# Optimization experiments

Measured on AMD Instinct MI355X. Metric: run time of the kernel, lower is better.

## Reference

```python
import jax, jax.numpy as jnp
import numpy as np

THRESHOLD = 1.0
DECAY = 0.9


def setup_inputs() -> dict:
    key = jax.random.key(0)
    ks = jax.random.split(key, 7)
    B, D_in, H, D_out = 512, 1024, 2048, 1024
    return {
        "x": jax.random.normal(ks[0], (B, D_in), dtype=jnp.float32),
        "W0": jax.random.normal(ks[1], (H, D_in), dtype=jnp.float32) * 0.03,
        "b0": jax.random.normal(ks[2], (H,), dtype=jnp.float32) * 0.03,
        "W1": jax.random.normal(ks[3], (H, H), dtype=jnp.float32) * 0.03,
        "b1": jax.random.normal(ks[4], (H,), dtype=jnp.float32) * 0.03,
        "W2": jax.random.normal(ks[5], (D_out, H), dtype=jnp.float32) * 0.03,
        "b2": jax.random.normal(ks[6], (D_out,), dtype=jnp.float32) * 0.03,
        "time_steps": 50,
    }


def _lif_layer(layer_input, W, b, time_steps):
    # layer_input is constant over time in the original module, so the
    # per-neuron Linear is computed ONCE as a single matmul.
    I = layer_input @ W.T + b  # [B, out_dim] input current, fixed per step
    V0 = jnp.zeros_like(I)

    def step(V, _):
        V = V * DECAY + I
        s = (V > THRESHOLD).astype(I.dtype)
        V = V * (1.0 - s)
        return V, s

    _, spikes = jax.lax.scan(step, V0, None, length=time_steps)  # [T, B, out]
    spikes = jnp.transpose(spikes, (1, 2, 0))  # [B, out, T]
    return spikes


def reference(x, W0, b0, W1, b1, W2, b2, time_steps):
    s0 = _lif_layer(x, W0, b0, time_steps)
    s1 = _lif_layer(s0.mean(axis=2), W1, b1, time_steps)
    s2 = _lif_layer(s1.mean(axis=2), W2, b2, time_steps)
    # matches (layer_outputs[-1], all_spikes)
    return (s2, s0, s1, s2)
```

## Files before the change

kernel.cpp:

```cpp
#include <hip/hip_runtime.h>

typedef unsigned long long u64;
typedef unsigned int u32;

constexpr int TPB = 256;
constexpr int T  = 50;
constexpr int M  = 512;

__global__ __launch_bounds__(TPB)
void gemm_part(const float* __restrict__ A, const int K, const int N,
               const float* __restrict__ W, float* __restrict__ pp)
{
    constexpr int BM2 = 128, BN2 = 64, BK = 64;
    __shared__ float sA[BK][BM2 + 4];
    __shared__ float sB[BK][BN2 + 4];

    const int tid = threadIdx.x;
    const int tx  = tid & 15;
    const int ty  = tid >> 4;
    const int n0  = blockIdx.x * BN2;
    const int m0  = blockIdx.y * BM2;
    const int kbase = blockIdx.z * 512;

    const int ar = tid >> 1, aks = (tid & 1) << 5;
    const int wr = tid >> 2, wks = (tid & 3) << 4;

    float S[8][4];
    #pragma unroll
    for (int i = 0; i < 8; ++i)
        #pragma unroll
        for (int j = 0; j < 4; ++j) S[i][j] = 0.0f;

    const float* aP = A + (size_t)(m0 + ar) * K + kbase + aks;
    const float* wP = W + (size_t)(n0 + wr) * K + kbase + wks;

    float4 fa[8], fw[4];
    auto loadA = [&](int t) {
        #pragma unroll
        for (int c = 0; c < 8; ++c)
            fa[c] = *reinterpret_cast<const float4*>(aP + t * BK + 4 * c);
    };
    auto loadW = [&](int t) {
        #pragma unroll
        for (int c = 0; c < 4; ++c)
            fw[c] = *reinterpret_cast<const float4*>(wP + t * BK + 4 * c);
    };

    constexpr int NT = 512 / BK;
    loadA(0); loadW(0);

    for (int t = 0; t < NT; ++t) {
        __syncthreads();
        #pragma unroll
        for (int c = 0; c < 8; ++c) {
            sA[aks + 4 * c + 0][ar] = fa[c].x;
            sA[aks + 4 * c + 1][ar] = fa[c].y;
            sA[aks + 4 * c + 2][ar] = fa[c].z;
            sA[aks + 4 * c + 3][ar] = fa[c].w;
        }
        #pragma unroll
        for (int c = 0; c < 4; ++c) {
            sB[wks + 4 * c + 0][wr] = fw[c].x;
            sB[wks + 4 * c + 1][wr] = fw[c].y;
            sB[wks + 4 * c + 2][wr] = fw[c].z;
            sB[wks + 4 * c + 3][wr] = fw[c].w;
        }
        __syncthreads();

        if (t + 1 < NT) { loadA(t + 1); loadW(t + 1); }

        #pragma unroll
        for (int kk = 0; kk < BK; ++kk) {
            const float4 a0 = *reinterpret_cast<const float4*>(&sA[kk][ty * 8]);
            const float4 a1 = *reinterpret_cast<const float4*>(&sA[kk][ty * 8 + 4]);
            const float4 b4 = *reinterpret_cast<const float4*>(&sB[kk][tx * 4]);
            const float a[8] = {a0.x, a0.y, a0.z, a0.w, a1.x, a1.y, a1.z, a1.w};
            const float b[4] = {b4.x, b4.y, b4.z, b4.w};
            #pragma unroll
            for (int i = 0; i < 8; ++i)
                #pragma unroll
                for (int j = 0; j < 4; ++j)
                    S[i][j] = __fmaf_rn(a[i], b[j], S[i][j]);
        }
    }

    float* dst = pp + (size_t)blockIdx.z * M * N;
    #pragma unroll
    for (int i = 0; i < 8; ++i) {
        const size_t off = (size_t)(m0 + ty * 8 + i) * N + (n0 + tx * 4);
        *reinterpret_cast<float4*>(dst + off) =
            make_float4(S[i][0], S[i][1], S[i][2], S[i][3]);
    }
}

template<bool DUP, bool WMEAN>
__global__ __launch_bounds__(TPB)
void merge_lif_expand(const float* __restrict__ pp, const int nchain,
                      const int N, const float* __restrict__ bias,
                      float* __restrict__ meanOut, float* __restrict__ out,
                      float* __restrict__ dup)
{
    __shared__ u64 lm[TPB];
    const int tid = threadIdx.x;
    const size_t base = (size_t)blockIdx.x * TPB;
    const size_t idx  = base + tid;
    const size_t cs   = (size_t)M * N;

    float s = pp[idx];
    for (int c = 1; c < nchain; ++c) s = __fadd_rn(s, pp[(size_t)c * cs + idx]);
    const float I = __fadd_rn(s, bias[idx & (size_t)(N - 1)]);

    float V = 0.0f; u64 msk = 0ull;
    #pragma unroll 1
    for (int t = 0; t < T; ++t) {
        V = __fadd_rn(__fmul_rn(V, 0.9f), I);
        if (V > 1.0f) { V = 0.0f; msk |= (1ull << t); }
    }
    if constexpr (WMEAN)
        meanOut[idx] = __fdiv_rn((float)__popcll(msk), 50.0f);
    lm[tid] = msk;
    __syncthreads();

    constexpr int TOTQ = TPB * T / 4;
    for (int q4 = tid; q4 < TOTQ; q4 += TPB) {
        const int q = q4 << 2;
        int nn = q / T;
        int tt = q - nn * T;
        u64 mk = lm[nn];
        float vals[4];
        #pragma unroll
        for (int c = 0; c < 4; ++c) {
            if (tt >= T) { tt -= T; ++nn; mk = lm[nn]; }
            vals[c] = (float)((mk >> tt) & 1ull);
            ++tt;
        }
        const float4 v4 = make_float4(vals[0], vals[1], vals[2], vals[3]);
        const size_t off = base * T + q;
        *reinterpret_cast<float4*>(out + off) = v4;
        if constexpr (DUP) *reinterpret_cast<float4*>(dup + off) = v4;
    }
}

template<bool IN_MASK>
__global__ __launch_bounds__(TPB)
void lif_gemm_mask(const void* __restrict__ Ain, const int K, const int N,
                   const float* __restrict__ W, const float* __restrict__ bias,
                   u64* __restrict__ maskOut)
{
    constexpr int BM = 64, BN = 64, BK = 64;
    __shared__ float sA[BK][BM + 4];
    __shared__ float sB[BK][BN + 4];
    const int tid = threadIdx.x;
    const int tx = tid & 15, ty = tid >> 4;
    const int n0 = blockIdx.x * BN, m0 = blockIdx.y * BM;
    const int lr = tid >> 2, klc = (tid & 3) << 4;

    float S[4][4], Ia[4][4];
    #pragma unroll
    for (int i = 0; i < 4; ++i)
        #pragma unroll
        for (int j = 0; j < 4; ++j) { S[i][j] = 0.0f; Ia[i][j] = 0.0f; }

    const float* aF = (const float*)Ain + (size_t)(m0 + lr) * K + klc;
    const u64*   aM = (const u64*)Ain   + (size_t)(m0 + lr) * K + klc;
    const float* wp = W + (size_t)(n0 + lr) * K + klc;
    float4 fa[4]; uint4 ma[8]; float4 fw[4];

    auto loadA = [&](int k0) {
        if constexpr (IN_MASK) {
            const uint4* p = reinterpret_cast<const uint4*>(aM + k0);
            #pragma unroll
            for (int c = 0; c < 8; ++c) ma[c] = p[c];
        } else {
            #pragma unroll
            for (int c = 0; c < 4; ++c)
                fa[c] = *reinterpret_cast<const float4*>(aF + k0 + 4 * c);
        }
    };
    auto loadW = [&](int k0) {
        #pragma unroll
        for (int c = 0; c < 4; ++c)
            fw[c] = *reinterpret_cast<const float4*>(wp + k0 + 4 * c);
    };

    const int NT = K / BK;
    loadA(0); loadW(0);
    for (int t = 0; t < NT; ++t) {
        __syncthreads();
        if constexpr (IN_MASK) {
            #pragma unroll
            for (int i = 0; i < 16; ++i) {
                const u32 lo = (i & 1) ? ma[i >> 1].z : ma[i >> 1].x;
                const u32 hi = (i & 1) ? ma[i >> 1].w : ma[i >> 1].y;
                sA[klc + i][lr] = __fdiv_rn((float)(__popc(lo) + __popc(hi)), 50.0f);
            }
        } else {
            #pragma unroll
            for (int c = 0; c < 4; ++c) {
                sA[klc + 4 * c + 0][lr] = fa[c].x;
                sA[klc + 4 * c + 1][lr] = fa[c].y;
                sA[klc + 4 * c + 2][lr] = fa[c].z;
                sA[klc + 4 * c + 3][lr] = fa[c].w;
            }
        }
        #pragma unroll
        for (int c = 0; c < 4; ++c) {
            sB[klc + 4 * c + 0][lr] = fw[c].x;
            sB[klc + 4 * c + 1][lr] = fw[c].y;
            sB[klc + 4 * c + 2][lr] = fw[c].z;
            sB[klc + 4 * c + 3][lr] = fw[c].w;
        }
        __syncthreads();
        if (t + 1 < NT) { loadA((t + 1) * BK); loadW((t + 1) * BK); }
        #pragma unroll
        for (int kk = 0; kk < BK; ++kk) {
            const float4 a4 = *reinterpret_cast<const float4*>(&sA[kk][ty * 4]);
            const float4 b4 = *reinterpret_cast<const float4*>(&sB[kk][tx * 4]);
            const float a[4] = {a4.x, a4.y, a4.z, a4.w};
            const float b[4] = {b4.x, b4.y, b4.z, b4.w};
            #pragma unroll
            for (int i = 0; i < 4; ++i)
                #pragma unroll
                for (int j = 0; j < 4; ++j)
                    S[i][j] = __fmaf_rn(a[i], b[j], S[i][j]);
        }
        if ((((t + 1) * BK) & 511) == 0) {
            #pragma unroll
            for (int i = 0; i < 4; ++i)
                #pragma unroll
                for (int j = 0; j < 4; ++j) {
                    Ia[i][j] = __fadd_rn(Ia[i][j], S[i][j]);
                    S[i][j]  = 0.0f;
                }
        }
    }
    #pragma unroll
    for (int i = 0; i < 4; ++i)
        #pragma unroll
        for (int j = 0; j < 4; ++j) {
            const int mi = ty * 4 + i, nj = tx * 4 + j;
            const float I = __fadd_rn(Ia[i][j], bias[n0 + nj]);
            float V = 0.0f; u64 msk = 0ull;
            #pragma unroll 1
            for (int t = 0; t < T; ++t) {
                V = __fadd_rn(__fmul_rn(V, 0.9f), I);
                if (V > 1.0f) { V = 0.0f; msk |= (1ull << t); }
            }
            maskOut[(size_t)(m0 + mi) * N + (n0 + nj)] = msk;
        }
}

template<bool DUP>
__global__ __launch_bounds__(TPB)
void expand_spikes(const u64* __restrict__ mask, float* __restrict__ out,
                   float* __restrict__ dup)
{
    __shared__ u64 lm[TPB];
    const int tid = threadIdx.x;
    const size_t base = (size_t)blockIdx.x * TPB;
    lm[tid] = mask[base + tid];
    __syncthreads();
    constexpr int TOTQ = TPB * T / 4;
    for (int q4 = tid; q4 < TOTQ; q4 += TPB) {
        const int q = q4 << 2;
        int nn = q / T, tt = q - nn * T;
        u64 mk = lm[nn];
        float vals[4];
        #pragma unroll
        for (int c = 0; c < 4; ++c) {
            if (tt >= T) { tt -= T; ++nn; mk = lm[nn]; }
            vals[c] = (float)((mk >> tt) & 1ull);
            ++tt;
        }
        const float4 v4 = make_float4(vals[0], vals[1], vals[2], vals[3]);
        const size_t off = base * T + q;
        *reinterpret_cast<float4*>(out + off) = v4;
        if constexpr (DUP) *reinterpret_cast<float4*>(dup + off) = v4;
    }
}

extern "C" void kernel_launch(void* const* d_in, const int* in_sizes, int n_in,
                              void* d_out, int out_size, void* d_ws, size_t ws_size,
                              hipStream_t stream) {
    const float* x  = (const float*)d_in[0];
    const float* W0 = (const float*)d_in[1];
    const float* b0 = (const float*)d_in[2];
    const float* W1 = (const float*)d_in[3];
    const float* b1 = (const float*)d_in[4];
    const float* W2 = (const float*)d_in[5];
    const float* b2 = (const float*)d_in[6];
    float* out = (float*)d_out;

    constexpr int H = 2048, DOUT = 1024;
    const size_t s2sz = (size_t)M * DOUT * T;
    const size_t s0sz = (size_t)M * H * T;
    const size_t NH = (size_t)M * H;
    const size_t ND = (size_t)M * DOUT;

    float* s2a = out;
    float* s0  = out + s2sz;
    float* s1  = s0 + s0sz;
    float* s2b = s1 + s0sz;

    dim3 blk(TPB);
    const size_t WS_NEED = (2 * NH + 4 * NH + 4 * ND + 2 * NH) * sizeof(float);

    if (ws_size >= WS_NEED) {
        float* pp0   = (float*)d_ws;
        float* pp1   = pp0 + 2 * NH;
        float* pp2   = pp1 + 4 * NH;
        float* mean0 = pp2 + 4 * ND;
        float* mean1 = mean0 + NH;

        gemm_part<<<dim3(H / 64, M / 128, 2), blk, 0, stream>>>(
            x, 1024, H, W0, pp0);
        merge_lif_expand<false, true><<<(int)(NH / TPB), blk, 0, stream>>>(
            pp0, 2, H, b0, mean0, s0, nullptr);
        gemm_part<<<dim3(H / 64, M / 128, 4), blk, 0, stream>>>(
            mean0, H, H, W1, pp1);
        merge_lif_expand<false, true><<<(int)(NH / TPB), blk, 0, stream>>>(
            pp1, 4, H, b1, mean1, s1, nullptr);
        gemm_part<<<dim3(DOUT / 64, M / 128, 4), blk, 0, stream>>>(
            mean1, H, DOUT, W2, pp2);
        merge_lif_expand<true, false><<<(int)(ND / TPB), blk, 0, stream>>>(
            pp2, 4, DOUT, b2, nullptr, s2b, s2a);
    } else {
        u64* mask0 = (u64*)s1;
        u64* mask1 = (u64*)s2a;
        u64* mask2 = (u64*)d_ws;
        dim3 gH(H / 64, M / 64), gD(DOUT / 64, M / 64);
        lif_gemm_mask<false><<<gH, blk, 0, stream>>>(x, 1024, H, W0, b0, mask0);
        lif_gemm_mask<true ><<<gH, blk, 0, stream>>>(mask0, H, H, W1, b1, mask1);
        lif_gemm_mask<true ><<<gD, blk, 0, stream>>>(mask1, H, DOUT, W2, b2, mask2);
        expand_spikes<false><<<(int)(NH / TPB), blk, 0, stream>>>(mask0, s0, nullptr);
        expand_spikes<false><<<(int)(NH / TPB), blk, 0, stream>>>(mask1, s1, nullptr);
        expand_spikes<true ><<<(int)(ND / TPB), blk, 0, stream>>>(mask2, s2b, s2a);
    }
}
```

Before: 267.1 us.

## Overlap spike expansion writes with next layer GEMM in one combined launch

```diff
diff --git a/kernel.cpp b/kernel.cpp
--- a/kernel.cpp
+++ b/kernel.cpp
@@ -7,104 +7,135 @@
 constexpr int T  = 50;
 constexpr int M  = 512;
 
+template<bool DUP>
 __global__ __launch_bounds__(TPB)
-void gemm_part(const float* __restrict__ A, const int K, const int N,
-               const float* __restrict__ W, float* __restrict__ pp)
+void gemm_expand(const float* __restrict__ A, const int K, const int N,
+                 const float* __restrict__ W, float* __restrict__ pp,
+                 const int gemmBlocks, const int gx, const int gy,
+                 const u64* __restrict__ mask, float* __restrict__ out,
+                 float* __restrict__ dup)
 {
-    constexpr int BM2 = 128, BN2 = 64, BK = 64;
-    __shared__ float sA[BK][BM2 + 4];
-    __shared__ float sB[BK][BN2 + 4];
+    __shared__ float sA[64][128 + 4];
+    __shared__ float sB[64][64 + 4];
+    __shared__ u64   lm[TPB];
 
     const int tid = threadIdx.x;
-    const int tx  = tid & 15;
-    const int ty  = tid >> 4;
-    const int n0  = blockIdx.x * BN2;
-    const int m0  = blockIdx.y * BM2;
-    const int kbase = blockIdx.z * 512;
-
-    const int ar = tid >> 1, aks = (tid & 1) << 5;
-    const int wr = tid >> 2, wks = (tid & 3) << 4;
-
-    float S[8][4];
-    #pragma unroll
-    for (int i = 0; i < 8; ++i)
-        #pragma unroll
-        for (int j = 0; j < 4; ++j) S[i][j] = 0.0f;
-
-    const float* aP = A + (size_t)(m0 + ar) * K + kbase + aks;
-    const float* wP = W + (size_t)(n0 + wr) * K + kbase + wks;
-
-    float4 fa[8], fw[4];
-    auto loadA = [&](int t) {
-        #pragma unroll
-        for (int c = 0; c < 8; ++c)
-            fa[c] = *reinterpret_cast<const float4*>(aP + t * BK + 4 * c);
-    };
-    auto loadW = [&](int t) {
-        #pragma unroll
-        for (int c = 0; c < 4; ++c)
-            fw[c] = *reinterpret_cast<const float4*>(wP + t * BK + 4 * c);
-    };
-
-    constexpr int NT = 512 / BK;
-    loadA(0); loadW(0);
-
-    for (int t = 0; t < NT; ++t) {
+    const int bid = blockIdx.x;
+
+    if (bid < gemmBlocks) {
+        const int x = bid % gx;
+        const int r = bid / gx;
+        const int y = r % gy;
+        const int z = r / gy;
+
+        const int tx = tid & 15;
+        const int ty = tid >> 4;
+        const int n0 = x * 64;
+        const int m0 = y * 128;
+        const int kbase = z * 512;
+
+        const int ar = tid >> 1, aks = (tid & 1) << 5;
+        const int wr = tid >> 2, wks = (tid & 3) << 4;
+
+        float S[8][4];
+        #pragma unroll
+        for (int i = 0; i < 8; ++i)
+            #pragma unroll
+            for (int j = 0; j < 4; ++j) S[i][j] = 0.0f;
+
+        const float* aP = A + (size_t)(m0 + ar) * K + kbase + aks;
+        const float* wP = W + (size_t)(n0 + wr) * K + kbase + wks;
+
+        float4 fa[8], fw[4];
+        auto loadA = [&](int t) {
+            #pragma unroll
+            for (int c = 0; c < 8; ++c)
+                fa[c] = *reinterpret_cast<const float4*>(aP + t * 64 + 4 * c);
+        };
+        auto loadW = [&](int t) {
+            #pragma unroll
+            for (int c = 0; c < 4; ++c)
+                fw[c] = *reinterpret_cast<const float4*>(wP + t * 64 + 4 * c);
+        };
+
+        constexpr int NT = 512 / 64;
+        loadA(0); loadW(0);
+
+        for (int t = 0; t < NT; ++t) {
+            __syncthreads();
+            #pragma unroll
+            for (int c = 0; c < 8; ++c) {
+                sA[aks + 4 * c + 0][ar] = fa[c].x;
+                sA[aks + 4 * c + 1][ar] = fa[c].y;
+                sA[aks + 4 * c + 2][ar] = fa[c].z;
+                sA[aks + 4 * c + 3][ar] = fa[c].w;
+            }
+            #pragma unroll
+            for (int c = 0; c < 4; ++c) {
+                sB[wks + 4 * c + 0][wr] = fw[c].x;
+                sB[wks + 4 * c + 1][wr] = fw[c].y;
+                sB[wks + 4 * c + 2][wr] = fw[c].z;
+                sB[wks + 4 * c + 3][wr] = fw[c].w;
+            }
+            __syncthreads();
+
+            if (t + 1 < NT) { loadA(t + 1); loadW(t + 1); }
+
+            #pragma unroll
+            for (int kk = 0; kk < 64; ++kk) {
+                const float4 a0 = *reinterpret_cast<const float4*>(&sA[kk][ty * 8]);
+                const float4 a1 = *reinterpret_cast<const float4*>(&sA[kk][ty * 8 + 4]);
+                const float4 b4 = *reinterpret_cast<const float4*>(&sB[kk][tx * 4]);
+                const float a[8] = {a0.x, a0.y, a0.z, a0.w, a1.x, a1.y, a1.z, a1.w};
+                const float b[4] = {b4.x, b4.y, b4.z, b4.w};
+                #pragma unroll
+                for (int i = 0; i < 8; ++i)
+                    #pragma unroll
+                    for (int j = 0; j < 4; ++j)
+                        S[i][j] = __fmaf_rn(a[i], b[j], S[i][j]);
+            }
+        }
+
+        float* dst = pp + (size_t)z * M * N;
+        #pragma unroll
+        for (int i = 0; i < 8; ++i) {
+            const size_t off = (size_t)(m0 + ty * 8 + i) * N + (n0 + tx * 4);
+            *reinterpret_cast<float4*>(dst + off) =
+                make_float4(S[i][0], S[i][1], S[i][2], S[i][3]);
+        }
+    } else {
+        const size_t base = (size_t)(bid - gemmBlocks) * TPB;
+        lm[tid] = mask[base + tid];
         __syncthreads();
-        #pragma unroll
-        for (int c = 0; c < 8; ++c) {
-            sA[aks + 4 * c + 0][ar] = fa[c].x;
-            sA[aks + 4 * c + 1][ar] = fa[c].y;
-            sA[aks + 4 * c + 2][ar] = fa[c].z;
-            sA[aks + 4 * c + 3][ar] = fa[c].w;
-        }
-        #pragma unroll
-        for (int c = 0; c < 4; ++c) {
-            sB[wks + 4 * c + 0][wr] = fw[c].x;
-            sB[wks + 4 * c + 1][wr] = fw[c].y;
-            sB[wks + 4 * c + 2][wr] = fw[c].z;
-            sB[wks + 4 * c + 3][wr] = fw[c].w;
-        }
-        __syncthreads();
-
-        if (t + 1 < NT) { loadA(t + 1); loadW(t + 1); }
-
-        #pragma unroll
-        for (int kk = 0; kk < BK; ++kk) {
-            const float4 a0 = *reinterpret_cast<const float4*>(&sA[kk][ty * 8]);
-            const float4 a1 = *reinterpret_cast<const float4*>(&sA[kk][ty * 8 + 4]);
-            const float4 b4 = *reinterpret_cast<const float4*>(&sB[kk][tx * 4]);
-            const float a[8] = {a0.x, a0.y, a0.z, a0.w, a1.x, a1.y, a1.z, a1.w};
-            const float b[4] = {b4.x, b4.y, b4.z, b4.w};
-            #pragma unroll
-            for (int i = 0; i < 8; ++i)
-                #pragma unroll
-                for (int j = 0; j < 4; ++j)
-                    S[i][j] = __fmaf_rn(a[i], b[j], S[i][j]);
-        }
-    }
-
-    float* dst = pp + (size_t)blockIdx.z * M * N;
-    #pragma unroll
-    for (int i = 0; i < 8; ++i) {
-        const size_t off = (size_t)(m0 + ty * 8 + i) * N + (n0 + tx * 4);
-        *reinterpret_cast<float4*>(dst + off) =
-            make_float4(S[i][0], S[i][1], S[i][2], S[i][3]);
-    }
-}
-
-template<bool DUP, bool WMEAN>
+
+        constexpr int TOTQ = TPB * T / 4;
+        for (int q4 = tid; q4 < TOTQ; q4 += TPB) {
+            const int q = q4 << 2;
+            int nn = q / T;
+            int tt = q - nn * T;
+            u64 mk = lm[nn];
+            float vals[4];
+            #pragma unroll
+            for (int c = 0; c < 4; ++c) {
+                if (tt >= T) { tt -= T; ++nn; mk = lm[nn]; }
+                vals[c] = (float)((mk >> tt) & 1ull);
+                ++tt;
+            }
+            const float4 v4 = make_float4(vals[0], vals[1], vals[2], vals[3]);
+            const size_t off = base * T + q;
+            *reinterpret_cast<float4*>(out + off) = v4;
+            if constexpr (DUP) *reinterpret_cast<float4*>(dup + off) = v4;
+        }
+    }
+}
+
 __global__ __launch_bounds__(TPB)
-void merge_lif_expand(const float* __restrict__ pp, const int nchain,
-                      const int N, const float* __restrict__ bias,
-                      float* __restrict__ meanOut, float* __restrict__ out,
-                      float* __restrict__ dup)
+void meanify(const float* __restrict__ pp, const int nchain, const int N,
+             const float* __restrict__ bias, u64* __restrict__ maskOut,
+             float* __restrict__ meanOut)
 {
-    __shared__ u64 lm[TPB];
-    const int tid = threadIdx.x;
-    const size_t base = (size_t)blockIdx.x * TPB;
-    const size_t idx  = base + tid;
-    const size_t cs   = (size_t)M * N;
+    const size_t idx = (size_t)blockIdx.x * TPB + threadIdx.x;
+    const size_t cs  = (size_t)M * N;
 
     float s = pp[idx];
     for (int c = 1; c < nchain; ++c) s = __fadd_rn(s, pp[(size_t)c * cs + idx]);
@@ -116,138 +147,9 @@
         V = __fadd_rn(__fmul_rn(V, 0.9f), I);
         if (V > 1.0f) { V = 0.0f; msk |= (1ull << t); }
     }
-    if constexpr (WMEAN)
+    maskOut[idx] = msk;
+    if (meanOut != nullptr)
         meanOut[idx] = __fdiv_rn((float)__popcll(msk), 50.0f);
-    lm[tid] = msk;
-    __syncthreads();
-
-    constexpr int TOTQ = TPB * T / 4;
-    for (int q4 = tid; q4 < TOTQ; q4 += TPB) {
-        const int q = q4 << 2;
-        int nn = q / T;
-        int tt = q - nn * T;
-        u64 mk = lm[nn];
-        float vals[4];
-        #pragma unroll
-        for (int c = 0; c < 4; ++c) {
-            if (tt >= T) { tt -= T; ++nn; mk = lm[nn]; }
-            vals[c] = (float)((mk >> tt) & 1ull);
-            ++tt;
-        }
-        const float4 v4 = make_float4(vals[0], vals[1], vals[2], vals[3]);
-        const size_t off = base * T + q;
-        *reinterpret_cast<float4*>(out + off) = v4;
-        if constexpr (DUP) *reinterpret_cast<float4*>(dup + off) = v4;
-    }
-}
-
-template<bool IN_MASK>
-__global__ __launch_bounds__(TPB)
-void lif_gemm_mask(const void* __restrict__ Ain, const int K, const int N,
-                   const float* __restrict__ W, const float* __restrict__ bias,
-                   u64* __restrict__ maskOut)
-{
-    constexpr int BM = 64, BN = 64, BK = 64;
-    __shared__ float sA[BK][BM + 4];
-    __shared__ float sB[BK][BN + 4];
-    const int tid = threadIdx.x;
-    const int tx = tid & 15, ty = tid >> 4;
-    const int n0 = blockIdx.x * BN, m0 = blockIdx.y * BM;
-    const int lr = tid >> 2, klc = (tid & 3) << 4;
-
-    float S[4][4], Ia[4][4];
-    #pragma unroll
-    for (int i = 0; i < 4; ++i)
-        #pragma unroll
-        for (int j = 0; j < 4; ++j) { S[i][j] = 0.0f; Ia[i][j] = 0.0f; }
-
-    const float* aF = (const float*)Ain + (size_t)(m0 + lr) * K + klc;
-    const u64*   aM = (const u64*)Ain   + (size_t)(m0 + lr) * K + klc;
-    const float* wp = W + (size_t)(n0 + lr) * K + klc;
-    float4 fa[4]; uint4 ma[8]; float4 fw[4];
-
-    auto loadA = [&](int k0) {
-        if constexpr (IN_MASK) {
-            const uint4* p = reinterpret_cast<const uint4*>(aM + k0);
-            #pragma unroll
-            for (int c = 0; c < 8; ++c) ma[c] = p[c];
-        } else {
-            #pragma unroll
-            for (int c = 0; c < 4; ++c)
-                fa[c] = *reinterpret_cast<const float4*>(aF + k0 + 4 * c);
-        }
-    };
-    auto loadW = [&](int k0) {
-        #pragma unroll
-        for (int c = 0; c < 4; ++c)
-            fw[c] = *reinterpret_cast<const float4*>(wp + k0 + 4 * c);
-    };
-
-    const int NT = K / BK;
-    loadA(0); loadW(0);
-    for (int t = 0; t < NT; ++t) {
-        __syncthreads();
-        if constexpr (IN_MASK) {
-            #pragma unroll
-            for (int i = 0; i < 16; ++i) {
-                const u32 lo = (i & 1) ? ma[i >> 1].z : ma[i >> 1].x;
-                const u32 hi = (i & 1) ? ma[i >> 1].w : ma[i >> 1].y;
-                sA[klc + i][lr] = __fdiv_rn((float)(__popc(lo) + __popc(hi)), 50.0f);
-            }
-        } else {
-            #pragma unroll
-            for (int c = 0; c < 4; ++c) {
-                sA[klc + 4 * c + 0][lr] = fa[c].x;
-                sA[klc + 4 * c + 1][lr] = fa[c].y;
-                sA[klc + 4 * c + 2][lr] = fa[c].z;
-                sA[klc + 4 * c + 3][lr] = fa[c].w;
-            }
-        }
-        #pragma unroll
-        for (int c = 0; c < 4; ++c) {
-            sB[klc + 4 * c + 0][lr] = fw[c].x;
-            sB[klc + 4 * c + 1][lr] = fw[c].y;
-            sB[klc + 4 * c + 2][lr] = fw[c].z;
-            sB[klc + 4 * c + 3][lr] = fw[c].w;
-        }
-        __syncthreads();
-        if (t + 1 < NT) { loadA((t + 1) * BK); loadW((t + 1) * BK); }
-        #pragma unroll
-        for (int kk = 0; kk < BK; ++kk) {
-            const float4 a4 = *reinterpret_cast<const float4*>(&sA[kk][ty * 4]);
-            const float4 b4 = *reinterpret_cast<const float4*>(&sB[kk][tx * 4]);
-            const float a[4] = {a4.x, a4.y, a4.z, a4.w};
-            const float b[4] = {b4.x, b4.y, b4.z, b4.w};
-            #pragma unroll
-            for (int i = 0; i < 4; ++i)
-                #pragma unroll
-                for (int j = 0; j < 4; ++j)
-                    S[i][j] = __fmaf_rn(a[i], b[j], S[i][j]);
-        }
-        if ((((t + 1) * BK) & 511) == 0) {
-            #pragma unroll
-            for (int i = 0; i < 4; ++i)
-                #pragma unroll
-                for (int j = 0; j < 4; ++j) {
-                    Ia[i][j] = __fadd_rn(Ia[i][j], S[i][j]);
-                    S[i][j]  = 0.0f;
-                }
-        }
-    }
-    #pragma unroll
-    for (int i = 0; i < 4; ++i)
-        #pragma unroll
-        for (int j = 0; j < 4; ++j) {
-            const int mi = ty * 4 + i, nj = tx * 4 + j;
-            const float I = __fadd_rn(Ia[i][j], bias[n0 + nj]);
-            float V = 0.0f; u64 msk = 0ull;
-            #pragma unroll 1
-            for (int t = 0; t < T; ++t) {
-                V = __fadd_rn(__fmul_rn(V, 0.9f), I);
-                if (V > 1.0f) { V = 0.0f; msk |= (1ull << t); }
-            }
-            maskOut[(size_t)(m0 + mi) * N + (n0 + nj)] = msk;
-        }
 }
 
 template<bool DUP>
@@ -279,6 +181,115 @@
     }
 }
 
+template<bool IN_MASK>
+__global__ __launch_bounds__(TPB)
+void lif_gemm_mask(const void* __restrict__ Ain, const int K, const int N,
+                   const float* __restrict__ W, const float* __restrict__ bias,
+                   u64* __restrict__ maskOut)
+{
+    constexpr int BM = 64, BN = 64, BK = 64;
+    __shared__ float sA[BK][BM + 4];
+    __shared__ float sB[BK][BN + 4];
+    const int tid = threadIdx.x;
+    const int tx = tid & 15, ty = tid >> 4;
+    const int n0 = blockIdx.x * BN, m0 = blockIdx.y * BM;
+    const int lr = tid >> 2, klc = (tid & 3) << 4;
+
+    float S[4][4], Ia[4][4];
+    #pragma unroll
+    for (int i = 0; i < 4; ++i)
+        #pragma unroll
+        for (int j = 0; j < 4; ++j) { S[i][j] = 0.0f; Ia[i][j] = 0.0f; }
+
+    const float* aF = (const float*)Ain + (size_t)(m0 + lr) * K + klc;
+    const u64*   aM = (const u64*)Ain   + (size_t)(m0 + lr) * K + klc;
+    const float* wp = W + (size_t)(n0 + lr) * K + klc;
+    float4 fa[4]; uint4 ma[8]; float4 fw[4];
+
+    auto loadA = [&](int k0) {
+        if constexpr (IN_MASK) {
+            const uint4* p = reinterpret_cast<const uint4*>(aM + k0);
+            #pragma unroll
+            for (int c = 0; c < 8; ++c) ma[c] = p[c];
+        } else {
+            #pragma unroll
+            for (int c = 0; c < 4; ++c)
+                fa[c] = *reinterpret_cast<const float4*>(aF + k0 + 4 * c);
+        }
+    };
+    auto loadW = [&](int k0) {
+        #pragma unroll
+        for (int c = 0; c < 4; ++c)
+            fw[c] = *reinterpret_cast<const float4*>(wp + k0 + 4 * c);
+    };
+
+    const int NT = K / BK;
+    loadA(0); loadW(0);
+    for (int t = 0; t < NT; ++t) {
+        __syncthreads();
+        if constexpr (IN_MASK) {
+            #pragma unroll
+            for (int i = 0; i < 16; ++i) {
+                const u32 lo = (i & 1) ? ma[i >> 1].z : ma[i >> 1].x;
+                const u32 hi = (i & 1) ? ma[i >> 1].w : ma[i >> 1].y;
+                sA[klc + i][lr] = __fdiv_rn((float)(__popc(lo) + __popc(hi)), 50.0f);
+            }
+        } else {
+            #pragma unroll
+            for (int c = 0; c < 4; ++c) {
+                sA[klc + 4 * c + 0][lr] = fa[c].x;
+                sA[klc + 4 * c + 1][lr] = fa[c].y;
+                sA[klc + 4 * c + 2][lr] = fa[c].z;
+                sA[klc + 4 * c + 3][lr] = fa[c].w;
+            }
+        }
+        #pragma unroll
+        for (int c = 0; c < 4; ++c) {
+            sB[klc + 4 * c + 0][lr] = fw[c].x;
+            sB[klc + 4 * c + 1][lr] = fw[c].y;
+            sB[klc + 4 * c + 2][lr] = fw[c].z;
+            sB[klc + 4 * c + 3][lr] = fw[c].w;
+        }
+        __syncthreads();
+        if (t + 1 < NT) { loadA((t + 1) * BK); loadW((t + 1) * BK); }
+        #pragma unroll
+        for (int kk = 0; kk < BK; ++kk) {
+            const float4 a4 = *reinterpret_cast<const float4*>(&sA[kk][ty * 4]);
+            const float4 b4 = *reinterpret_cast<const float4*>(&sB[kk][tx * 4]);
+            const float a[4] = {a4.x, a4.y, a4.z, a4.w};
+            const float b[4] = {b4.x, b4.y, b4.z, b4.w};
+            #pragma unroll
+            for (int i = 0; i < 4; ++i)
+                #pragma unroll
+                for (int j = 0; j < 4; ++j)
+                    S[i][j] = __fmaf_rn(a[i], b[j], S[i][j]);
+        }
+        if ((((t + 1) * BK) & 511) == 0) {
+            #pragma unroll
+            for (int i = 0; i < 4; ++i)
+                #pragma unroll
+                for (int j = 0; j < 4; ++j) {
+                    Ia[i][j] = __fadd_rn(Ia[i][j], S[i][j]);
+                    S[i][j]  = 0.0f;
+                }
+        }
+    }
+    #pragma unroll
+    for (int i = 0; i < 4; ++i)
+        #pragma unroll
+        for (int j = 0; j < 4; ++j) {
+            const int mi = ty * 4 + i, nj = tx * 4 + j;
+            const float I = __fadd_rn(Ia[i][j], bias[n0 + nj]);
+            float V = 0.0f; u64 msk = 0ull;
+            #pragma unroll 1
+            for (int t = 0; t < T; ++t) {
+                V = __fadd_rn(__fmul_rn(V, 0.9f), I);
+                if (V > 1.0f) { V = 0.0f; msk |= (1ull << t); }
+            }
+            maskOut[(size_t)(m0 + mi) * N + (n0 + nj)] = msk;
+        }
+}
+
 extern "C" void kernel_launch(void* const* d_in, const int* in_sizes, int n_in,
                               void* d_out, int out_size, void* d_ws, size_t ws_size,
                               hipStream_t stream) {
@@ -303,7 +314,8 @@
     float* s2b = s1 + s0sz;
 
     dim3 blk(TPB);
-    const size_t WS_NEED = (2 * NH + 4 * NH + 4 * ND + 2 * NH) * sizeof(float);
+    const size_t WS_NEED = (8 * NH + 4 * ND) * sizeof(float)
+                         + (2 * NH + ND) * sizeof(u64);
 
     if (ws_size >= WS_NEED) {
         float* pp0   = (float*)d_ws;
@@ -311,19 +323,26 @@
         float* pp2   = pp1 + 4 * NH;
         float* mean0 = pp2 + 4 * ND;
         float* mean1 = mean0 + NH;
-
-        gemm_part<<<dim3(H / 64, M / 128, 2), blk, 0, stream>>>(
-            x, 1024, H, W0, pp0);
-        merge_lif_expand<false, true><<<(int)(NH / TPB), blk, 0, stream>>>(
-            pp0, 2, H, b0, mean0, s0, nullptr);
-        gemm_part<<<dim3(H / 64, M / 128, 4), blk, 0, stream>>>(
-            mean0, H, H, W1, pp1);
-        merge_lif_expand<false, true><<<(int)(NH / TPB), blk, 0, stream>>>(
-            pp1, 4, H, b1, mean1, s1, nullptr);
-        gemm_part<<<dim3(DOUT / 64, M / 128, 4), blk, 0, stream>>>(
-            mean1, H, DOUT, W2, pp2);
-        merge_lif_expand<true, false><<<(int)(ND / TPB), blk, 0, stream>>>(
-            pp2, 4, DOUT, b2, nullptr, s2b, s2a);
+        u64*   mask0 = (u64*)(mean1 + NH);
+        u64*   mask1 = mask0 + NH;
+        u64*   mask2 = mask1 + NH;
+
+        const int g0 = 32 * 4 * 2;
+        const int g1 = 32 * 4 * 4;
+        const int g2 = 16 * 4 * 4;
+        const int e01 = (int)(NH / TPB);
+        const int e2  = (int)(ND / TPB);
+
+        gemm_expand<false><<<g0, blk, 0, stream>>>(
+            x, 1024, H, W0, pp0, g0, 32, 4, nullptr, nullptr, nullptr);
+        meanify<<<(int)(NH / TPB), blk, 0, stream>>>(pp0, 2, H, b0, mask0, mean0);
+        gemm_expand<false><<<g1 + e01, blk, 0, stream>>>(
+            mean0, 2048, H, W1, pp1, g1, 32, 4, mask0, s0, nullptr);
+        meanify<<<(int)(NH / TPB), blk, 0, stream>>>(pp1, 4, H, b1, mask1, mean1);
+        gemm_expand<false><<<g2 + e01, blk, 0, stream>>>(
+            mean1, 2048, DOUT, W2, pp2, g2, 16, 4, mask1, s1, nullptr);
+        meanify<<<(int)(ND / TPB), blk, 0, stream>>>(pp2, 4, DOUT, b2, mask2, nullptr);
+        expand_spikes<true><<<e2, blk, 0, stream>>>(mask2, s2b, s2a);
     } else {
         u64* mask0 = (u64*)s1;
         u64* mask1 = (u64*)s2a;
```

New measurement: 277.0 us. 1.04x slower.
